# Kernel optimization log

Measured on AMD Instinct MI355X. Metric: run time of the kernel, lower is better.

## Reference

```python
import jax, jax.numpy as jnp
import numpy as np

B, CIN, H, W = 4, 256, 56, 56
COUT, K = 256, 3
STRIDE, PAD, OG = 1, 1, 1
KK = K * K


def setup_inputs() -> dict:
    key = jax.random.key(0)
    k1, k2, k3, k4 = jax.random.split(key, 4)
    x = jax.random.normal(k1, (B, CIN, H, W), jnp.float32)
    # deformable conv weight [Cout, Cin/groups, K, K]
    weight = jax.random.normal(k2, (COUT, CIN, K, K), jnp.float32) * 0.05
    # offset-predicting 3x3 conv: 2*OG*K*K output channels (small init -> modest offsets)
    off_w = jax.random.normal(k3, (2 * OG * KK, CIN, 3, 3), jnp.float32) * 0.01
    off_b = jax.random.normal(k4, (2 * OG * KK,), jnp.float32) * 0.01
    return {"x": x, "weight": weight, "off_w": off_w, "off_b": off_b}


def _deform_conv(x, weight, off_w, off_b):
    Bn, C, Hh, Ww = x.shape
    # offset = param_generator(x): 3x3 conv, stride 1, pad 1
    offset = jax.lax.conv_general_dilated(
        x, off_w, window_strides=(1, 1), padding=((1, 1), (1, 1)),
        dimension_numbers=("NCHW", "OIHW", "NCHW")) + off_b[None, :, None, None]
    Ho = (Hh + 2 * PAD - K) // STRIDE + 1
    Wo = (Ww + 2 * PAD - K) // STRIDE + 1
    # torchvision layout: [B, OG, KK, (dy,dx), Ho, Wo]
    off = offset.reshape(Bn, OG, KK, 2, Ho, Wo)

    kh = jnp.arange(KK) // K
    kw = jnp.arange(KK) % K
    base_y = (jnp.arange(Ho) * STRIDE - PAD)[None, :, None] + kh[:, None, None]  # [KK,Ho,1]
    base_x = (jnp.arange(Wo) * STRIDE - PAD)[None, None, :] + kw[:, None, None]  # [KK,1,Wo]
    py = base_y[None, None].astype(x.dtype) + off[:, :, :, 0]  # [B,OG,KK,Ho,Wo]
    px = base_x[None, None].astype(x.dtype) + off[:, :, :, 1]

    Cg = C // OG
    xg = x.reshape(Bn, OG, Cg, Hh * Ww)

    def gather(yc, xc, wgt):
        # zero-padded bilinear corner: out-of-bounds samples contribute 0
        valid = (yc >= 0) & (yc < Hh) & (xc >= 0) & (xc < Ww)
        idx = (jnp.clip(yc, 0, Hh - 1) * Ww + jnp.clip(xc, 0, Ww - 1)).reshape(Bn, OG, 1, -1)
        v = jnp.take_along_axis(xg, idx, axis=3)            # [B,OG,Cg,KK*Ho*Wo]
        w = (wgt * valid.astype(wgt.dtype)).reshape(Bn, OG, 1, -1)
        return v * w

    y0 = jnp.floor(py).astype(jnp.int32)
    x0 = jnp.floor(px).astype(jnp.int32)
    ty = py - y0
    tx = px - x0
    sampled = (gather(y0,     x0,     (1 - ty) * (1 - tx))
             + gather(y0,     x0 + 1, (1 - ty) * tx)
             + gather(y0 + 1, x0,     ty * (1 - tx))
             + gather(y0 + 1, x0 + 1, ty * tx))
    sampled = sampled.reshape(Bn, C, KK, Ho, Wo)
    # weighted accumulation: implicit GEMM over (Cin, KK)
    return jnp.einsum("bikhw,oik->bohw", sampled, weight.reshape(COUT, C, KK))


def reference(x, weight, off_w, off_b):
    return _deform_conv(x, weight, off_w, off_b)
```

## Files before the change

### kernel.cpp

```cpp
#include <hip/hip_runtime.h>
#include <hip/hip_bf16.h>

#define B_N   4
#define CIN_  256
#define HH_   56
#define WW_   56
#define COUT_ 256
#define KK_   9
#define HW_   3136
#define KDIM  2304
#define NOFF  (B_N*18*HW_)
#define NOUT  (B_N*COUT_*HW_)

typedef __attribute__((ext_vector_type(8))) short short8;
typedef __attribute__((ext_vector_type(4))) float float4v;

__device__ __forceinline__ short f2bf_bits(float v) {
    union { __hip_bfloat16 h; short s; } u;
    u.h = __float2bfloat16(v);
    return u.s;
}
__device__ __forceinline__ float bfbits2f(short s) {
    union { unsigned u; float f; } u2;
    u2.u = ((unsigned)(unsigned short)s) << 16;
    return u2.f;
}

#define NB_AT  2304
#define NB_XT  784
#define NB_OW3 288
__global__ __launch_bounds__(256) void k_front(const float* __restrict__ x,
                                               const float* __restrict__ wgt,
                                               const float* __restrict__ ow,
                                               short* __restrict__ At,
                                               short* __restrict__ xTb,
                                               short* __restrict__ owT3) {
    __shared__ float tile[64][65];
    int bx = blockIdx.x;
    int t = threadIdx.x;
    if (bx < NB_AT) {
        int i = bx*256 + t;
        int o = i / KDIM; int r = i % KDIM;
        int kk = r >> 8;  int ci = r & 255;
        At[i] = f2bf_bits(wgt[(size_t)(o*CIN_ + ci)*9 + kk]);
        return;
    }
    if (bx < NB_AT + NB_XT) {
        int g = bx - NB_AT;
        int b = g / 196; int r = g % 196;
        int c0 = (r / 49) * 64; int p0 = (r % 49) * 64;
        int tp = t & 63;  int tc = t >> 6;
        #pragma unroll
        for (int i = 0; i < 16; ++i) {
            int ci = tc*16 + i;
            tile[ci][tp] = x[((size_t)b*CIN_ + c0 + ci)*HW_ + p0 + tp];
        }
        __syncthreads();
        #pragma unroll
        for (int i = 0; i < 16; ++i) {
            int p = tc*16 + i;
            xTb[((size_t)b*HW_ + p0 + p)*CIN_ + c0 + tp] = f2bf_bits(tile[tp][p]);
        }
        return;
    }
    {
        int i = (bx - NB_AT - NB_XT)*256 + t;
        int c = i / KDIM; int r = i % KDIM;
        int kk = r >> 8;  int ci = r & 255;
        owT3[i] = (c < 18) ? f2bf_bits(ow[(size_t)(c*CIN_ + ci)*9 + kk]) : 0;
    }
}

__global__ __launch_bounds__(256) void k_offgemm(const short* __restrict__ owT3,
                                                 const short* __restrict__ xTb,
                                                 float* __restrict__ pOff2) {
    __shared__ short sA[32*64];
    __shared__ short sB[64*64];
    __shared__ int   sP2[3*64];
    int t = threadIdx.x;
    int posb = blockIdx.x * 64;
    int b    = blockIdx.y;
    int ks   = blockIdx.z;
    int kt0  = ks * 768;
    int kend = kt0 + 768;

    for (int e = t; e < 3*64; e += 256) {
        int kk = ks*3 + (e >> 6); int row = e & 63;
        int pos = posb + row;
        int h = pos / WW_, w = pos % WW_;
        int yy = h + kk/3 - 1, xx = w + kk%3 - 1;
        bool v = (yy >= 0) && (yy < HH_) && (xx >= 0) && (xx < WW_);
        sP2[e] = v ? (yy*WW_ + xx) : -1;
    }
    __syncthreads();

    int arow = t >> 3,  aq  = t & 7;
    int brow = t >> 2,  bqc = (t & 3) * 2;

    int wv = t >> 6;
    int wm = (wv >> 1) * 16;
    int wn = (wv & 1) * 32;
    int lane = t & 63;
    int lm = lane & 15;
    int qd = lane >> 4;

    float4v acc[2];
    acc[0] = (float4v)(0.f); acc[1] = (float4v)(0.f);

    const short* gA = owT3 + (size_t)arow*KDIM + aq*8;
    const short* xb = xTb + (size_t)b*HW_*CIN_;

    short* wA = sA + (((arow >> 4)*8 + aq)*16 + ((arow + 2*aq) & 15))*8;
    short* wB[2];
    #pragma unroll
    for (int j = 0; j < 2; ++j) {
        int qq = bqc + j;
        wB[j] = sB + (((brow >> 4)*8 + qq)*16 + ((brow + 2*qq) & 15))*8;
    }

    short8 pa, pb[2];
    const short8 zero8 = (short8)(0);
    pa = *(const short8*)(gA + kt0);
    {
        int p2 = sP2[brow];
        #pragma unroll
        for (int j = 0; j < 2; ++j) {
            int ci0 = (kt0 & 255) + (bqc + j)*8;
            pb[j] = (p2 >= 0) ? *(const short8*)(xb + (size_t)p2*CIN_ + ci0) : zero8;
        }
    }

    for (int kt = kt0; kt < kend; kt += 64) {
        __syncthreads();
        *(short8*)wA = pa;
        #pragma unroll
        for (int j = 0; j < 2; ++j) *(short8*)wB[j] = pb[j];
        __syncthreads();
        int kt2 = kt + 64;
        if (kt2 < kend) {
            pa = *(const short8*)(gA + kt2);
            int kkl = (kt2 >> 8) - ks*3;
            int p2 = sP2[kkl*64 + brow];
            int cb = kt2 & 255;
            #pragma unroll
            for (int j = 0; j < 2; ++j) {
                int ci0 = cb + (bqc + j)*8;
                pb[j] = (p2 >= 0) ? *(const short8*)(xb + (size_t)p2*CIN_ + ci0) : zero8;
            }
        }
        #pragma unroll
        for (int kss = 0; kss < 2; ++kss) {
            int qe = kss*4 + qd;
            int sw = (lm + 2*qe) & 15;
            short8 af, bf[2];
            af = *(short8*)(sA + ((((wm>>4))*8 + qe)*16 + sw)*8);
            #pragma unroll
            for (int j = 0; j < 2; ++j)
                bf[j] = *(short8*)(sB + ((((wn>>4) + j)*8 + qe)*16 + sw)*8);
            #pragma unroll
            for (int j = 0; j < 2; ++j)
                acc[j] = __builtin_amdgcn_mfma_f32_16x16x32_bf16(
                             af, bf[j], acc[j], 0, 0, 0);
        }
    }

    float* pbase = pOff2 + (size_t)ks*NOFF;
    #pragma unroll
    for (int j = 0; j < 2; ++j) {
        int col = posb + wn + j*16 + lm;
        #pragma unroll
        for (int r = 0; r < 4; ++r) {
            int c = wm + qd*4 + r;
            if (c < 18)
                pbase[((size_t)(b*18 + c))*HW_ + col] = acc[j][r];
        }
    }
}

__global__ __launch_bounds__(256) void k_gemm(const short* __restrict__ At,
                                              const short* __restrict__ xTb,
                                              const float* __restrict__ pOff2,
                                              const float* __restrict__ ob,
                                              float* __restrict__ out) {
    __shared__ short sA[128*64];
    __shared__ short sB[64*64];
    __shared__ int4   sPI[3*64];
    __shared__ float4 sPW[3*64];
    int t = threadIdx.x;

    int idx = blockIdx.x;
    int xcd = idx & 7;
    int b   = xcd & 3;
    int q   = (idx >> 3)*2 + (xcd >> 2);
    int m0   = (q & 1) * 128;
    int r2   = q >> 1;
    int posb = (r2 % 49) * 64;
    int ks   = r2 / 49;
    int kt0  = ks * 768;
    int kend = kt0 + 768;

    for (int e = t; e < 3*64; e += 256) {
        int kk = ks*3 + (e >> 6); int pl = e & 63;
        int pos = posb + pl;
        int h = pos / WW_, w = pos % WW_;
        size_t oy = (size_t)(b*18 + 2*kk    )*HW_ + pos;
        size_t ox = (size_t)(b*18 + 2*kk + 1)*HW_ + pos;
        float dy = ob[2*kk], dx = ob[2*kk + 1];
        #pragma unroll
        for (int s = 0; s < 3; ++s) {
            dy += pOff2[(size_t)s*NOFF + oy];
            dx += pOff2[(size_t)s*NOFF + ox];
        }
        float py = (float)(h - 1 + kk/3) + dy;
        float px = (float)(w - 1 + kk%3) + dx;
        float y0f = floorf(py), x0f = floorf(px);
        int y0 = (int)y0f, x0 = (int)x0f;
        float ty = py - y0f, tx = px - x0f;
        bool vy0 = (y0   >= 0) && (y0   < HH_);
        bool vy1 = (y0+1 >= 0) && (y0+1 < HH_);
        bool vx0 = (x0   >= 0) && (x0   < WW_);
        bool vx1 = (x0+1 >= 0) && (x0+1 < WW_);
        int y0c = min(max(y0,   0), HH_-1), y1c = min(max(y0+1, 0), HH_-1);
        int x0c = min(max(x0,   0), WW_-1), x1c = min(max(x0+1, 0), WW_-1);
        sPI[e] = make_int4(y0c*WW_+x0c, y0c*WW_+x1c, y1c*WW_+x0c, y1c*WW_+x1c);
        sPW[e] = make_float4((vy0 && vx0) ? (1.f-ty)*(1.f-tx) : 0.f,
                             (vy0 && vx1) ? (1.f-ty)*tx       : 0.f,
                             (vy1 && vx0) ? ty*(1.f-tx)       : 0.f,
                             (vy1 && vx1) ? ty*tx             : 0.f);
    }
    __syncthreads();

    int arow = t >> 1,  aqc = (t & 1) * 4;
    int brow = t >> 2,  bqc = (t & 3) * 2;

    int wv = t >> 6;
    int wm = (wv >> 1) * 64;
    int wn = (wv & 1) * 32;
    int lane = t & 63;
    int lm = lane & 15;
    int qd = lane >> 4;

    float4v acc[4][2];
    #pragma unroll
    for (int i = 0; i < 4; ++i)
        #pragma unroll
        for (int j = 0; j < 2; ++j) acc[i][j] = (float4v)(0.f);

    const short* gA = At + (size_t)(m0 + arow)*KDIM + aqc*8;
    const short* xb = xTb + (size_t)b*HW_*CIN_;

    short* wA[4]; short* wB[2];
    #pragma unroll
    for (int j = 0; j < 4; ++j) {
        int qq = aqc + j;
        wA[j] = sA + (((arow >> 4)*8 + qq)*16 + ((arow + 2*qq) & 15))*8;
    }
    #pragma unroll
    for (int j = 0; j < 2; ++j) {
        int qq = bqc + j;
        wB[j] = sB + (((brow >> 4)*8 + qq)*16 + ((brow + 2*qq) & 15))*8;
    }

    short8 pa[4], cg[2][4];
    float4 bwv;
    #pragma unroll
    for (int j = 0; j < 4; ++j) pa[j] = *(const short8*)(gA + kt0 + j*8);
    {
        int4 id = sPI[brow]; bwv = sPW[brow];
        #pragma unroll
        for (int j = 0; j < 2; ++j) {
            int ci0 = (bqc + j)*8;
            cg[j][0] = *(const short8*)(xb + (size_t)id.x*CIN_ + ci0);
            cg[j][1] = *(const short8*)(xb + (size_t)id.y*CIN_ + ci0);
            cg[j][2] = *(const short8*)(xb + (size_t)id.z*CIN_ + ci0);
            cg[j][3] = *(const short8*)(xb + (size_t)id.w*CIN_ + ci0);
        }
    }

    for (int kt = kt0; kt < kend; kt += 64) {
        short8 pk[2];
        #pragma unroll
        for (int j = 0; j < 2; ++j) {
            float f[8];
            #pragma unroll
            for (int e = 0; e < 8; ++e)
                f[e] = bwv.x*bfbits2f(cg[j][0][e]) + bwv.y*bfbits2f(cg[j][1][e])
                     + bwv.z*bfbits2f(cg[j][2][e]) + bwv.w*bfbits2f(cg[j][3][e]);
            union { short8 s8; __hip_bfloat162 h2[4]; } pu;
            #pragma unroll
            for (int e2 = 0; e2 < 4; ++e2)
                pu.h2[e2] = __float22bfloat162_rn(make_float2(f[2*e2], f[2*e2+1]));
            pk[j] = pu.s8;
        }
        __syncthreads();
        #pragma unroll
        for (int j = 0; j < 4; ++j) *(short8*)wA[j] = pa[j];
        #pragma unroll
        for (int j = 0; j < 2; ++j) *(short8*)wB[j] = pk[j];
        __syncthreads();
        int kt2 = kt + 64;
        if (kt2 < kend) {
            #pragma unroll
            for (int j = 0; j < 4; ++j) pa[j] = *(const short8*)(gA + kt2 + j*8);
            int kkl = (kt2 >> 8) - ks*3;
            int4 id = sPI[kkl*64 + brow]; bwv = sPW[kkl*64 + brow];
            int cb = kt2 & 255;
            #pragma unroll
            for (int j = 0; j < 2; ++j) {
                int ci0 = cb + (bqc + j)*8;
                cg[j][0] = *(const short8*)(xb + (size_t)id.x*CIN_ + ci0);
                cg[j][1] = *(const short8*)(xb + (size_t)id.y*CIN_ + ci0);
                cg[j][2] = *(const short8*)(xb + (size_t)id.z*CIN_ + ci0);
                cg[j][3] = *(const short8*)(xb + (size_t)id.w*CIN_ + ci0);
            }
        }
        #pragma unroll
        for (int kss = 0; kss < 2; ++kss) {
            int qe = kss*4 + qd;
            int sw = (lm + 2*qe) & 15;
            short8 af[4], bf[2];
            #pragma unroll
            for (int i = 0; i < 4; ++i)
                af[i] = *(short8*)(sA + ((((wm>>4) + i)*8 + qe)*16 + sw)*8);
            #pragma unroll
            for (int j = 0; j < 2; ++j)
                bf[j] = *(short8*)(sB + ((((wn>>4) + j)*8 + qe)*16 + sw)*8);
            #pragma unroll
            for (int i = 0; i < 4; ++i)
                #pragma unroll
                for (int j = 0; j < 2; ++j)
                    acc[i][j] = __builtin_amdgcn_mfma_f32_16x16x32_bf16(
                                    af[i], bf[j], acc[i][j], 0, 0, 0);
        }
    }

    #pragma unroll
    for (int i = 0; i < 4; ++i)
        #pragma unroll
        for (int j = 0; j < 2; ++j) {
            int col = posb + wn + j*16 + lm;
            #pragma unroll
            for (int r = 0; r < 4; ++r) {
                int m = m0 + wm + i*16 + qd*4 + r;
                unsafeAtomicAdd(&out[((size_t)b*COUT_ + m)*HW_ + col], acc[i][j][r]);
            }
        }
}

extern "C" void kernel_launch(void* const* d_in, const int* in_sizes, int n_in,
                              void* d_out, int out_size, void* d_ws, size_t ws_size,
                              hipStream_t stream) {
    const float* x   = (const float*)d_in[0];
    const float* wgt = (const float*)d_in[1];
    const float* ow  = (const float*)d_in[2];
    const float* ob  = (const float*)d_in[3];
    float* out = (float*)d_out;

    char* ws = (char*)d_ws;
    short* At    = (short*)ws;
    short* xTb   = (short*)(ws + 1179648);
    short* owT3  = (short*)(ws + 7602176);
    float* pOff2 = (float*)(ws + 7749632);

    hipMemsetAsync(out, 0, (size_t)NOUT*4, stream);
    k_front  <<<dim3(NB_AT + NB_XT + NB_OW3), 256, 0, stream>>>(x, wgt, ow, At, xTb, owT3);
    k_offgemm<<<dim3(49, 4, 3),               256, 0, stream>>>(owT3, xTb, pOff2);
    k_gemm   <<<dim3(1176),                   256, 0, stream>>>(At, xTb, pOff2, ob, out);
}
```

Measured before the change: 144.2 us.

## Double-buffer gather prefetch and replace atomic split-K output with partial-sum reduce

The main GEMM loop is now fully unrolled over 12 K-steps. The bilinear-corner gathers use two alternating register buffers, so each gather is issued two iterations ahead of its use, which deepens latency hiding for the irregular loads. The split-K atomics into a memset output are replaced by plain stores into three partial buffers in workspace, followed by a new reduce kernel that sums them. This removes the memset and atomic contention, but adds roughly 38 MB of extra write-then-read traffic, one more launch, and more register pressure.

```diff
diff --git a/kernel.cpp b/kernel.cpp
--- a/kernel.cpp
+++ b/kernel.cpp
@@ -181,7 +181,7 @@
                                               const short* __restrict__ xTb,
                                               const float* __restrict__ pOff2,
                                               const float* __restrict__ ob,
-                                              float* __restrict__ out) {
+                                              float* __restrict__ pout) {
     __shared__ short sA[128*64];
     __shared__ short sB[64*64];
     __shared__ int4   sPI[3*64];
@@ -197,7 +197,6 @@
     int posb = (r2 % 49) * 64;
     int ks   = r2 / 49;
     int kt0  = ks * 768;
-    int kend = kt0 + 768;
 
     for (int e = t; e < 3*64; e += 256) {
         int kk = ks*3 + (e >> 6); int pl = e & 63;
@@ -261,79 +260,87 @@
         wB[j] = sB + (((brow >> 4)*8 + qq)*16 + ((brow + 2*qq) & 15))*8;
     }
 
-    short8 pa[4], cg[2][4];
-    float4 bwv;
-    #pragma unroll
-    for (int j = 0; j < 4; ++j) pa[j] = *(const short8*)(gA + kt0 + j*8);
-    {
-        int4 id = sPI[brow]; bwv = sPW[brow];
-        #pragma unroll
-        for (int j = 0; j < 2; ++j) {
-            int ci0 = (bqc + j)*8;
-            cg[j][0] = *(const short8*)(xb + (size_t)id.x*CIN_ + ci0);
-            cg[j][1] = *(const short8*)(xb + (size_t)id.y*CIN_ + ci0);
-            cg[j][2] = *(const short8*)(xb + (size_t)id.z*CIN_ + ci0);
-            cg[j][3] = *(const short8*)(xb + (size_t)id.w*CIN_ + ci0);
-        }
-    }
-
-    for (int kt = kt0; kt < kend; kt += 64) {
-        short8 pk[2];
-        #pragma unroll
-        for (int j = 0; j < 2; ++j) {
-            float f[8];
-            #pragma unroll
-            for (int e = 0; e < 8; ++e)
-                f[e] = bwv.x*bfbits2f(cg[j][0][e]) + bwv.y*bfbits2f(cg[j][1][e])
-                     + bwv.z*bfbits2f(cg[j][2][e]) + bwv.w*bfbits2f(cg[j][3][e]);
-            union { short8 s8; __hip_bfloat162 h2[4]; } pu;
-            #pragma unroll
-            for (int e2 = 0; e2 < 4; ++e2)
-                pu.h2[e2] = __float22bfloat162_rn(make_float2(f[2*e2], f[2*e2+1]));
-            pk[j] = pu.s8;
-        }
-        __syncthreads();
-        #pragma unroll
-        for (int j = 0; j < 4; ++j) *(short8*)wA[j] = pa[j];
-        #pragma unroll
-        for (int j = 0; j < 2; ++j) *(short8*)wB[j] = pk[j];
-        __syncthreads();
-        int kt2 = kt + 64;
-        if (kt2 < kend) {
-            #pragma unroll
-            for (int j = 0; j < 4; ++j) pa[j] = *(const short8*)(gA + kt2 + j*8);
-            int kkl = (kt2 >> 8) - ks*3;
-            int4 id = sPI[kkl*64 + brow]; bwv = sPW[kkl*64 + brow];
-            int cb = kt2 & 255;
-            #pragma unroll
-            for (int j = 0; j < 2; ++j) {
-                int ci0 = cb + (bqc + j)*8;
-                cg[j][0] = *(const short8*)(xb + (size_t)id.x*CIN_ + ci0);
-                cg[j][1] = *(const short8*)(xb + (size_t)id.y*CIN_ + ci0);
-                cg[j][2] = *(const short8*)(xb + (size_t)id.z*CIN_ + ci0);
-                cg[j][3] = *(const short8*)(xb + (size_t)id.w*CIN_ + ci0);
-            }
-        }
-        #pragma unroll
-        for (int kss = 0; kss < 2; ++kss) {
-            int qe = kss*4 + qd;
-            int sw = (lm + 2*qe) & 15;
-            short8 af[4], bf[2];
-            #pragma unroll
-            for (int i = 0; i < 4; ++i)
-                af[i] = *(short8*)(sA + ((((wm>>4) + i)*8 + qe)*16 + sw)*8);
-            #pragma unroll
-            for (int j = 0; j < 2; ++j)
-                bf[j] = *(short8*)(sB + ((((wn>>4) + j)*8 + qe)*16 + sw)*8);
-            #pragma unroll
-            for (int i = 0; i < 4; ++i)
-                #pragma unroll
-                for (int j = 0; j < 2; ++j)
-                    acc[i][j] = __builtin_amdgcn_mfma_f32_16x16x32_bf16(
-                                    af[i], bf[j], acc[i][j], 0, 0, 0);
-        }
-    }
-
+    short8 pa[4];
+    short8 cgA[2][4], cgB[2][4];
+    float4 bwA, bwB;
+
+#define PALOAD(itX) do {                                                      \
+    _Pragma("unroll")                                                         \
+    for (int j = 0; j < 4; ++j)                                               \
+        pa[j] = *(const short8*)(gA + kt0 + (itX)*64 + j*8);                  \
+} while (0)
+
+#define CGLOAD(cg, bw, itX) do {                                              \
+    int4 id_ = sPI[((itX) >> 2)*64 + brow];                                   \
+    bw = sPW[((itX) >> 2)*64 + brow];                                         \
+    int cb_ = ((itX) & 3) * 64;                                               \
+    _Pragma("unroll")                                                         \
+    for (int j = 0; j < 2; ++j) {                                             \
+        int ci0_ = cb_ + (bqc + j)*8;                                         \
+        cg[j][0] = *(const short8*)(xb + (size_t)id_.x*CIN_ + ci0_);          \
+        cg[j][1] = *(const short8*)(xb + (size_t)id_.y*CIN_ + ci0_);          \
+        cg[j][2] = *(const short8*)(xb + (size_t)id_.z*CIN_ + ci0_);          \
+        cg[j][3] = *(const short8*)(xb + (size_t)id_.w*CIN_ + ci0_);          \
+    }                                                                         \
+} while (0)
+
+#define GSTEP(cg, bw, it) do {                                                \
+    short8 pk[2];                                                             \
+    _Pragma("unroll")                                                         \
+    for (int j = 0; j < 2; ++j) {                                             \
+        float f[8];                                                           \
+        _Pragma("unroll")                                                     \
+        for (int e = 0; e < 8; ++e)                                           \
+            f[e] = bw.x*bfbits2f(cg[j][0][e]) + bw.y*bfbits2f(cg[j][1][e])    \
+                 + bw.z*bfbits2f(cg[j][2][e]) + bw.w*bfbits2f(cg[j][3][e]);   \
+        union { short8 s8; __hip_bfloat162 h2[4]; } pu;                       \
+        _Pragma("unroll")                                                     \
+        for (int e2 = 0; e2 < 4; ++e2)                                        \
+            pu.h2[e2] = __float22bfloat162_rn(make_float2(f[2*e2], f[2*e2+1]));\
+        pk[j] = pu.s8;                                                        \
+    }                                                                         \
+    __syncthreads();                            \
+    _Pragma("unroll")                                                         \
+    for (int j = 0; j < 4; ++j) *(short8*)wA[j] = pa[j];                      \
+    _Pragma("unroll")                                                         \
+    for (int j = 0; j < 2; ++j) *(short8*)wB[j] = pk[j];                      \
+    __syncthreads();                                                          \
+    if ((it) + 1 < 12) PALOAD((it) + 1);                                      \
+    if ((it) + 2 < 12) CGLOAD(cg, bw, (it) + 2);                              \
+    _Pragma("unroll")                                                         \
+    for (int kss = 0; kss < 2; ++kss) {                                       \
+        int qe = kss*4 + qd;                                                  \
+        int sw = (lm + 2*qe) & 15;                                            \
+        short8 af[4], bf[2];                                                  \
+        _Pragma("unroll")                                                     \
+        for (int i = 0; i < 4; ++i)                                           \
+            af[i] = *(short8*)(sA + ((((wm>>4) + i)*8 + qe)*16 + sw)*8);      \
+        _Pragma("unroll")                                                     \
+        for (int j = 0; j < 2; ++j)                                           \
+            bf[j] = *(short8*)(sB + ((((wn>>4) + j)*8 + qe)*16 + sw)*8);      \
+        _Pragma("unroll")                                                     \
+        for (int i = 0; i < 4; ++i)                                           \
+            _Pragma("unroll")                                                 \
+            for (int j = 0; j < 2; ++j)                                       \
+                acc[i][j] = __builtin_amdgcn_mfma_f32_16x16x32_bf16(          \
+                                af[i], bf[j], acc[i][j], 0, 0, 0);            \
+    }                                                                         \
+} while (0)
+
+    PALOAD(0);
+    CGLOAD(cgA, bwA, 0);
+    CGLOAD(cgB, bwB, 1);
+
+    for (int it2 = 0; it2 < 6; ++it2) {
+        GSTEP(cgA, bwA, it2*2);
+        GSTEP(cgB, bwB, it2*2 + 1);
+    }
+
+#undef PALOAD
+#undef CGLOAD
+#undef GSTEP
+
+    float* pbase = pout + (size_t)ks*NOUT;
     #pragma unroll
     for (int i = 0; i < 4; ++i)
         #pragma unroll
@@ -342,9 +349,22 @@
             #pragma unroll
             for (int r = 0; r < 4; ++r) {
                 int m = m0 + wm + i*16 + qd*4 + r;
-                unsafeAtomicAdd(&out[((size_t)b*COUT_ + m)*HW_ + col], acc[i][j][r]);
+                pbase[((size_t)b*COUT_ + m)*HW_ + col] = acc[i][j][r];
             }
         }
+}
+
+__global__ __launch_bounds__(256) void k_oreduce(const float* __restrict__ pout,
+                                                 float* __restrict__ out) {
+    int i = blockIdx.x*256 + threadIdx.x;
+    if (i >= NOUT/4) return;
+    float4 a = ((const float4*)pout)[i];
+    float4 b = ((const float4*)(pout + NOUT))[i];
+    float4 c = ((const float4*)(pout + 2*(size_t)NOUT))[i];
+    float4 r;
+    r.x = a.x + b.x + c.x;  r.y = a.y + b.y + c.y;
+    r.z = a.z + b.z + c.z;  r.w = a.w + b.w + c.w;
+    ((float4*)out)[i] = r;
 }
 
 extern "C" void kernel_launch(void* const* d_in, const int* in_sizes, int n_in,
@@ -361,9 +381,10 @@
     short* xTb   = (short*)(ws + 1179648);
     short* owT3  = (short*)(ws + 7602176);
     float* pOff2 = (float*)(ws + 7749632);
-
-    hipMemsetAsync(out, 0, (size_t)NOUT*4, stream);
+    float* pout  = (float*)(ws + 10459136);
+
     k_front  <<<dim3(NB_AT + NB_XT + NB_OW3), 256, 0, stream>>>(x, wgt, ow, At, xTb, owT3);
     k_offgemm<<<dim3(49, 4, 3),               256, 0, stream>>>(owT3, xTb, pOff2);
-    k_gemm   <<<dim3(1176),                   256, 0, stream>>>(At, xTb, pOff2, ob, out);
-}
+    k_gemm   <<<dim3(1176),                   256, 0, stream>>>(At, xTb, pOff2, ob, pout);
+    k_oreduce<<<dim3(NOUT/4/256),             256, 0, stream>>>(pout, out);
+}
```

Result: faster. 137.9 us (-4.4%).

## Pre-swizzle weights into MFMA fragment layout and replace atomics with split-K reduce

Applied to the files above, without the earlier changes.

Weights are rewritten in the front kernel into a layout that matches the MFMA A-fragment order, so each wave loads its A operands straight from global memory into registers and the shared-memory A tile and its stores are removed. The three split-K partial outputs are now written to separate workspace buffers with plain stores instead of float atomics into a zeroed output, and a new reduce kernel sums them. This drops the memset and the atomic traffic, but adds an extra kernel and about 3x output-sized workspace writes and reads. A loads now come from global memory or L2 on every iteration without reuse through shared memory.

```diff
diff --git a/kernel.cpp b/kernel.cpp
--- a/kernel.cpp
+++ b/kernel.cpp
@@ -32,7 +32,7 @@
 __global__ __launch_bounds__(256) void k_front(const float* __restrict__ x,
                                                const float* __restrict__ wgt,
                                                const float* __restrict__ ow,
-                                               short* __restrict__ At,
+                                               short* __restrict__ At2,
                                                short* __restrict__ xTb,
                                                short* __restrict__ owT3) {
     __shared__ float tile[64][65];
@@ -40,9 +40,15 @@
     int t = threadIdx.x;
     if (bx < NB_AT) {
         int i = bx*256 + t;
-        int o = i / KDIM; int r = i % KDIM;
-        int kk = r >> 8;  int ci = r & 255;
-        At[i] = f2bf_bits(wgt[(size_t)(o*CIN_ + ci)*9 + kk]);
+        int e = i & 7;
+        int l = (i >> 3) & 63;
+        int gg = i >> 9;
+        int g  = gg % 72;
+        int rt = gg / 72;
+        int m = rt*16 + (l & 15);
+        int k = g*32 + (l >> 4)*8 + e;
+        int kk = k >> 8;  int ci = k & 255;
+        At2[i] = f2bf_bits(wgt[(size_t)(m*CIN_ + ci)*9 + kk]);
         return;
     }
     if (bx < NB_AT + NB_XT) {
@@ -177,12 +183,11 @@
     }
 }
 
-__global__ __launch_bounds__(256) void k_gemm(const short* __restrict__ At,
+__global__ __launch_bounds__(256) void k_gemm(const short* __restrict__ At2,
                                               const short* __restrict__ xTb,
                                               const float* __restrict__ pOff2,
                                               const float* __restrict__ ob,
-                                              float* __restrict__ out) {
-    __shared__ short sA[128*64];
+                                              float* __restrict__ pout) {
     __shared__ short sB[64*64];
     __shared__ int4   sPI[3*64];
     __shared__ float4 sPW[3*64];
@@ -196,8 +201,6 @@
     int r2   = q >> 1;
     int posb = (r2 % 49) * 64;
     int ks   = r2 / 49;
-    int kt0  = ks * 768;
-    int kend = kt0 + 768;
 
     for (int e = t; e < 3*64; e += 256) {
         int kk = ks*3 + (e >> 6); int pl = e & 63;
@@ -230,7 +233,6 @@
     }
     __syncthreads();
 
-    int arow = t >> 1,  aqc = (t & 1) * 4;
     int brow = t >> 2,  bqc = (t & 3) * 2;
 
     int wv = t >> 6;
@@ -246,38 +248,45 @@
         #pragma unroll
         for (int j = 0; j < 2; ++j) acc[i][j] = (float4v)(0.f);
 
-    const short* gA = At + (size_t)(m0 + arow)*KDIM + aqc*8;
     const short* xb = xTb + (size_t)b*HW_*CIN_;
-
-    short* wA[4]; short* wB[2];
-    #pragma unroll
-    for (int j = 0; j < 4; ++j) {
-        int qq = aqc + j;
-        wA[j] = sA + (((arow >> 4)*8 + qq)*16 + ((arow + 2*qq) & 15))*8;
-    }
+    const short* pA = At2 + (((size_t)((m0 + wm) >> 4) * 72) << 9) + (size_t)lane * 8;
+    int g0 = ks * 24;
+
+    short* wB[2];
     #pragma unroll
     for (int j = 0; j < 2; ++j) {
         int qq = bqc + j;
         wB[j] = sB + (((brow >> 4)*8 + qq)*16 + ((brow + 2*qq) & 15))*8;
     }
 
-    short8 pa[4], cg[2][4];
+    short8 cg[2][4];
     float4 bwv;
-    #pragma unroll
-    for (int j = 0; j < 4; ++j) pa[j] = *(const short8*)(gA + kt0 + j*8);
-    {
-        int4 id = sPI[brow]; bwv = sPW[brow];
-        #pragma unroll
-        for (int j = 0; j < 2; ++j) {
-            int ci0 = (bqc + j)*8;
-            cg[j][0] = *(const short8*)(xb + (size_t)id.x*CIN_ + ci0);
-            cg[j][1] = *(const short8*)(xb + (size_t)id.y*CIN_ + ci0);
-            cg[j][2] = *(const short8*)(xb + (size_t)id.z*CIN_ + ci0);
-            cg[j][3] = *(const short8*)(xb + (size_t)id.w*CIN_ + ci0);
-        }
-    }
-
-    for (int kt = kt0; kt < kend; kt += 64) {
+
+#define CGLOAD(itX) do {                                                      \
+    int4 id_ = sPI[((itX) >> 2)*64 + brow];                                   \
+    bwv = sPW[((itX) >> 2)*64 + brow];                                        \
+    int cb_ = ((itX) & 3) * 64;                                               \
+    _Pragma("unroll")                                                         \
+    for (int j = 0; j < 2; ++j) {                                             \
+        int ci0_ = cb_ + (bqc + j)*8;                                         \
+        cg[j][0] = *(const short8*)(xb + (size_t)id_.x*CIN_ + ci0_);          \
+        cg[j][1] = *(const short8*)(xb + (size_t)id_.y*CIN_ + ci0_);          \
+        cg[j][2] = *(const short8*)(xb + (size_t)id_.z*CIN_ + ci0_);          \
+        cg[j][3] = *(const short8*)(xb + (size_t)id_.w*CIN_ + ci0_);          \
+    }                                                                         \
+} while (0)
+
+    CGLOAD(0);
+
+    for (int it = 0; it < 12; ++it) {
+        short8 af[8];
+        #pragma unroll
+        for (int kss = 0; kss < 2; ++kss)
+            #pragma unroll
+            for (int i = 0; i < 4; ++i)
+                af[kss*4 + i] = *(const short8*)(
+                    pA + ((size_t)(i*72 + g0 + it*2 + kss) << 9));
+
         short8 pk[2];
         #pragma unroll
         for (int j = 0; j < 2; ++j) {
@@ -294,34 +303,15 @@
         }
         __syncthreads();
         #pragma unroll
-        for (int j = 0; j < 4; ++j) *(short8*)wA[j] = pa[j];
-        #pragma unroll
         for (int j = 0; j < 2; ++j) *(short8*)wB[j] = pk[j];
         __syncthreads();
-        int kt2 = kt + 64;
-        if (kt2 < kend) {
-            #pragma unroll
-            for (int j = 0; j < 4; ++j) pa[j] = *(const short8*)(gA + kt2 + j*8);
-            int kkl = (kt2 >> 8) - ks*3;
-            int4 id = sPI[kkl*64 + brow]; bwv = sPW[kkl*64 + brow];
-            int cb = kt2 & 255;
-            #pragma unroll
-            for (int j = 0; j < 2; ++j) {
-                int ci0 = cb + (bqc + j)*8;
-                cg[j][0] = *(const short8*)(xb + (size_t)id.x*CIN_ + ci0);
-                cg[j][1] = *(const short8*)(xb + (size_t)id.y*CIN_ + ci0);
-                cg[j][2] = *(const short8*)(xb + (size_t)id.z*CIN_ + ci0);
-                cg[j][3] = *(const short8*)(xb + (size_t)id.w*CIN_ + ci0);
-            }
-        }
+        if (it + 1 < 12) CGLOAD(it + 1);
+
         #pragma unroll
         for (int kss = 0; kss < 2; ++kss) {
             int qe = kss*4 + qd;
             int sw = (lm + 2*qe) & 15;
-            short8 af[4], bf[2];
-            #pragma unroll
-            for (int i = 0; i < 4; ++i)
-                af[i] = *(short8*)(sA + ((((wm>>4) + i)*8 + qe)*16 + sw)*8);
+            short8 bf[2];
             #pragma unroll
             for (int j = 0; j < 2; ++j)
                 bf[j] = *(short8*)(sB + ((((wn>>4) + j)*8 + qe)*16 + sw)*8);
@@ -330,10 +320,12 @@
                 #pragma unroll
                 for (int j = 0; j < 2; ++j)
                     acc[i][j] = __builtin_amdgcn_mfma_f32_16x16x32_bf16(
-                                    af[i], bf[j], acc[i][j], 0, 0, 0);
-        }
-    }
-
+                                    af[kss*4 + i], bf[j], acc[i][j], 0, 0, 0);
+        }
+    }
+#undef CGLOAD
+
+    float* pbase = pout + (size_t)ks*NOUT;
     #pragma unroll
     for (int i = 0; i < 4; ++i)
         #pragma unroll
@@ -342,9 +334,22 @@
             #pragma unroll
             for (int r = 0; r < 4; ++r) {
                 int m = m0 + wm + i*16 + qd*4 + r;
-                unsafeAtomicAdd(&out[((size_t)b*COUT_ + m)*HW_ + col], acc[i][j][r]);
+                pbase[((size_t)b*COUT_ + m)*HW_ + col] = acc[i][j][r];
             }
         }
+}
+
+__global__ __launch_bounds__(256) void k_oreduce(const float* __restrict__ pout,
+                                                 float* __restrict__ out) {
+    int i = blockIdx.x*256 + threadIdx.x;
+    if (i >= NOUT/4) return;
+    float4 a = ((const float4*)pout)[i];
+    float4 b = ((const float4*)(pout + NOUT))[i];
+    float4 c = ((const float4*)(pout + 2*(size_t)NOUT))[i];
+    float4 r;
+    r.x = a.x + b.x + c.x;  r.y = a.y + b.y + c.y;
+    r.z = a.z + b.z + c.z;  r.w = a.w + b.w + c.w;
+    ((float4*)out)[i] = r;
 }
 
 extern "C" void kernel_launch(void* const* d_in, const int* in_sizes, int n_in,
@@ -357,13 +362,14 @@
     float* out = (float*)d_out;
 
     char* ws = (char*)d_ws;
-    short* At    = (short*)ws;
+    short* At2   = (short*)ws;
     short* xTb   = (short*)(ws + 1179648);
     short* owT3  = (short*)(ws + 7602176);
     float* pOff2 = (float*)(ws + 7749632);
-
-    hipMemsetAsync(out, 0, (size_t)NOUT*4, stream);
-    k_front  <<<dim3(NB_AT + NB_XT + NB_OW3), 256, 0, stream>>>(x, wgt, ow, At, xTb, owT3);
+    float* pout  = (float*)(ws + 10459136);
+
+    k_front  <<<dim3(NB_AT + NB_XT + NB_OW3), 256, 0, stream>>>(x, wgt, ow, At2, xTb, owT3);
     k_offgemm<<<dim3(49, 4, 3),               256, 0, stream>>>(owT3, xTb, pOff2);
-    k_gemm   <<<dim3(1176),                   256, 0, stream>>>(At, xTb, pOff2, ob, out);
-}
+    k_gemm   <<<dim3(1176),                   256, 0, stream>>>(At2, xTb, pOff2, ob, pout);
+    k_oreduce<<<dim3(NOUT/4/256),             256, 0, stream>>>(pout, out);
+}
```

New measurement: 128.8 us. 10.7% less time.
